# Kernel tuning notes

Hardware: AMD Instinct MI355X
Metric: run time of the kernel (lower is better)

## Reference

```python
import jax, jax.numpy as jnp
import numpy as np
from jax import lax

N = 256
BATCH = 4096
N_MZIS = N * (N - 1) // 2  # 32640


def _reck_positions(n):
    # Static MZI position schedule: for layer in range(n-1): for pos in range(n-1-layer)
    return np.concatenate([np.arange(n - 1 - layer) for layer in range(n - 1)]).astype(np.int32)


def setup_inputs() -> dict:
    key = jax.random.key(0)
    k1, k2, k3, k4 = jax.random.split(key, 4)
    x = jax.random.normal(k1, (BATCH, N), dtype=jnp.float32)
    theta = jax.random.uniform(k2, (N_MZIS,), dtype=jnp.float32) * (np.pi / 2)
    phi_internal = jax.random.uniform(k3, (N_MZIS,), dtype=jnp.float32) * (2 * np.pi)
    phi_external = jax.random.uniform(k4, (N,), dtype=jnp.float32) * (2 * np.pi)
    return {"x": x, "theta": theta, "phi_internal": phi_internal, "phi_external": phi_external}


def _construct_unitary(theta, phi_internal, phi_external):
    n = phi_external.shape[0]
    positions = jnp.asarray(_reck_positions(n))  # [n_mzis], static schedule

    def step(U, inputs):
        pos, th, ph = inputs
        # Extract the two rows touched by this MZI and apply the 2x2 transfer matrix:
        # [[cos,          -sin*e^{-i phi}],
        #  [sin*e^{i phi}, cos          ]]
        rows = lax.dynamic_slice(U, (pos, jnp.int32(0)), (2, n))  # [2, n]
        r0, r1 = rows[0], rows[1]
        c = jnp.cos(th)
        s = jnp.sin(th)
        e = jnp.cos(ph) + 1j * jnp.sin(ph)
        new_rows = jnp.stack([c * r0 - s * jnp.conj(e) * r1,
                              s * e * r0 + c * r1])
        return lax.dynamic_update_slice(U, new_rows, (pos, jnp.int32(0))), None

    U0 = jnp.eye(n, dtype=jnp.complex64)
    U, _ = lax.scan(step, U0, (positions, theta, phi_internal))
    # Final external phase screen: diag(e^{i phi_ext}) @ U
    phase = jnp.cos(phi_external) + 1j * jnp.sin(phi_external)
    return phase[:, None] * U


def reference(x, theta, phi_internal, phi_external):
    U = _construct_unitary(theta, phi_internal, phi_external)  # [N, N] complex64
    out_c = x.astype(jnp.complex64) @ jnp.conj(U).T            # [B, N] complex64
    return jnp.real(out_c).astype(jnp.float32)
```

## Files before the change

### kernel.cpp

```cpp
#include <hip/hip_runtime.h>


#define NN 256
#define NB 4096

typedef float f32x4 __attribute__((ext_vector_type(4)));
typedef short bf16x8 __attribute__((ext_vector_type(8)));

#define WS_AT_OFF   0u
#define WS_BT_OFF   (512u * 1024u)
#define WS_CF_OFF   (1u << 20)
#define WS_PART_OFF (1u << 20)
#define WS_WB_OFF   (3u << 20)
#define WS_XB_OFF   ((3u << 20) + (1u << 19))

__device__ __forceinline__ unsigned short f2bf(float f) {
    unsigned u = __builtin_bit_cast(unsigned, f);
    unsigned r = (u + 0x7FFFu + ((u >> 16) & 1u)) >> 16;
    return (unsigned short)r;
}

__global__ __launch_bounds__(64) void coeff2_kernel(const float* __restrict__ theta,
                                                    const float* __restrict__ phi,
                                                    f32x4* __restrict__ cf3) {
    const int t = blockIdx.x;
    const int l = threadIdx.x;
    const int g = t >> 3, jj = t & 7;
    const int pA = (t & 1) ? (4 * l + 1) : (4 * l);
#pragma unroll
    for (int s = 0; s < 2; ++s) {
        int p = pA + 2 * s;
        f32x4 v = {1.f, 0.f, 0.f, 0.f};
        if (p <= t && p + t <= 508) {
            int L = (t - p) >> 1;
            int k = ((L * (511 - L)) >> 1) + p;
            float st, ct, sp, cp;
            __sincosf(theta[k], &st, &ct);
            __sincosf(phi[k], &sp, &cp);
            v = (f32x4){ct, st * cp, st * sp, 0.f};
        }
        cf3[(g * 16 + 8 * s + jj) * 64 + l] = v;
    }
}

__device__ __forceinline__ float dpp_up1(float x) {
    int r = __builtin_amdgcn_update_dpp(0, __builtin_bit_cast(int, x), 0x138, 0xF, 0xF, true);
    return __builtin_bit_cast(float, r);
}
__device__ __forceinline__ float dpp_dn1(float x) {
    int r = __builtin_amdgcn_update_dpp(0, __builtin_bit_cast(int, x), 0x130, 0xF, 0xF, true);
    return __builtin_bit_cast(float, r);
}

__device__ __forceinline__ void rot2(float& ar, float& ai, float& br, float& bi, f32x4 co) {
    float c = co.x, sx = co.y, sy = co.z;
    float nar = c * ar - (sx * br + sy * bi);
    float nai = c * ai - (sx * bi - sy * br);
    float nbr = sx * ar - sy * ai + c * br;
    float nbi = sx * ai + sy * ar + c * bi;
    ar = nar; ai = nai; br = nbr; bi = nbi;
}

__device__ __forceinline__ void fence() {
    asm volatile("" ::: "memory");
    __builtin_amdgcn_sched_barrier(0);
}

__global__ __launch_bounds__(64, 1) void build_kernel(const f32x4* __restrict__ cf3,
                                                      float2* __restrict__ Ata,
                                                      float2* __restrict__ Btb) {
    const int l  = threadIdx.x;
    const int r0 = 4 * l;
    const int j  = blockIdx.x;
    const int h  = blockIdx.y;
    const int G0 = 32 * h;
    float2* dst = (h ? Ata : Btb) + (size_t)j * NN;

    float ur0 = (r0 + 0 == j) ? 1.f : 0.f, ui0 = 0.f;
    float ur1 = (r0 + 1 == j) ? 1.f : 0.f, ui1 = 0.f;
    float ur2 = (r0 + 2 == j) ? 1.f : 0.f, ui2 = 0.f;
    float ur3 = (r0 + 3 == j) ? 1.f : 0.f, ui3 = 0.f;
    const float lane0_one = (l == 0) ? 1.f : 0.f;

    f32x4 RA[16], RB[16];

    auto loadgrp = [&](int g, f32x4 (&R)[16]) {
        const f32x4* sp = cf3 + (size_t)g * 1024 + l;
#pragma unroll
        for (int s = 0; s < 16; ++s) R[s] = sp[s * 64];
    };

    auto compute = [&](const f32x4 (&R)[16]) {
#pragma unroll
        for (int jj = 0; jj < 8; ++jj) {
            if ((jj & 1) == 0) {
                rot2(ur0, ui0, ur1, ui1, R[jj]);
                rot2(ur2, ui2, ur3, ui3, R[8 + jj]);
            } else {
                float d0r = dpp_dn1(ur0), d0i = dpp_dn1(ui0);
                float u3r = dpp_up1(ur3), u3i = dpp_up1(ui3);
                f32x4 cb = R[8 + jj];
                float cx = dpp_up1(cb.x) + lane0_one;
                float cy = dpp_up1(cb.y);
                float cz = dpp_up1(cb.z);
                rot2(ur1, ui1, ur2, ui2, R[jj]);
                float n3r = cb.x * ur3 - (cb.y * d0r + cb.z * d0i);
                float n3i = cb.x * ui3 - (cb.y * d0i - cb.z * d0r);
                float n0r = cy * u3r - cz * u3i + cx * ur0;
                float n0i = cy * u3i + cz * u3r + cx * ui0;
                ur3 = n3r; ui3 = n3i; ur0 = n0r; ui0 = n0i;
            }
        }
    };

    loadgrp(G0 + 0, RA);
    fence();
    for (int g = 0; g < 32; g += 2) {
        if (g + 1 < 32) loadgrp(G0 + g + 1, RB);
        fence();
        compute(RA);
        if (g + 2 < 32) loadgrp(G0 + g + 2, RA);
        fence();
        compute(RB);
    }

    *(float4*)(dst + r0)     = make_float4(ur0, ui0, ur1, ui1);
    *(float4*)(dst + r0 + 2) = make_float4(ur2, ui2, ur3, ui3);
}

__global__ __launch_bounds__(256) void merge_part_kernel(const float2* __restrict__ At,
                                                         const float2* __restrict__ Bt,
                                                         float2* __restrict__ parts) {
    __shared__ float2 Ats[32][36];
    __shared__ float2 Bts[32][36];

    const int t  = threadIdx.x;
    const int i0 = blockIdx.x * 32;
    const int j0 = blockIdx.y * 32;
    const int kc0 = blockIdx.z * 64;
    const int ti = (t & 15) * 2;
    const int tj = (t >> 4) * 2;

    float sr00 = 0, si00 = 0, sr01 = 0, si01 = 0;
    float sr10 = 0, si10 = 0, sr11 = 0, si11 = 0;

    for (int kc = kc0; kc < kc0 + 64; kc += 32) {
#pragma unroll
        for (int rep = 0; rep < 2; ++rep) {
            int e  = t + rep * 256;
            int kk = e >> 4;
            int f4 = e & 15;
            float4 v = *(const float4*)(At + (size_t)(kc + kk) * NN + i0 + 2 * f4);
            Ats[kk][2 * f4]     = make_float2(v.x, v.y);
            Ats[kk][2 * f4 + 1] = make_float2(v.z, v.w);
            float4 w = *(const float4*)(Bt + (size_t)(j0 + kk) * NN + kc + 2 * f4);
            Bts[kk][2 * f4]     = make_float2(w.x, w.y);
            Bts[kk][2 * f4 + 1] = make_float2(w.z, w.w);
        }
        __syncthreads();
#pragma unroll 8
        for (int k = 0; k < 32; ++k) {
            float2 a0 = Ats[k][ti], a1 = Ats[k][ti + 1];
            float2 b0 = Bts[tj][k], b1 = Bts[tj + 1][k];
            sr00 += a0.x * b0.x - a0.y * b0.y;  si00 += a0.x * b0.y + a0.y * b0.x;
            sr01 += a1.x * b0.x - a1.y * b0.y;  si01 += a1.x * b0.y + a1.y * b0.x;
            sr10 += a0.x * b1.x - a0.y * b1.y;  si10 += a0.x * b1.y + a0.y * b1.x;
            sr11 += a1.x * b1.x - a1.y * b1.y;  si11 += a1.x * b1.y + a1.y * b1.x;
        }
        __syncthreads();
    }

    float2* p = parts + (size_t)blockIdx.z * (NN * NN);
    p[(size_t)(i0 + ti) * NN + j0 + tj]         = make_float2(sr00, si00);
    p[(size_t)(i0 + ti + 1) * NN + j0 + tj]     = make_float2(sr01, si01);
    p[(size_t)(i0 + ti) * NN + j0 + tj + 1]     = make_float2(sr10, si10);
    p[(size_t)(i0 + ti + 1) * NN + j0 + tj + 1] = make_float2(sr11, si11);
}

__global__ __launch_bounds__(256) void reduce_kernel(const float2* __restrict__ parts,
                                                     const float* __restrict__ phi_ext,
                                                     unsigned short* __restrict__ Wb) {
    int gid = blockIdx.x * 256 + threadIdx.x;
    int i  = gid >> 6;
    int j  = (gid & 63) * 4;
    float re0 = 0, im0 = 0, re1 = 0, im1 = 0, re2 = 0, im2 = 0, re3 = 0, im3 = 0;
#pragma unroll
    for (int z = 0; z < 4; ++z) {
        const float2* p = parts + (size_t)z * (NN * NN) + (size_t)i * NN + j;
        float4 a = *(const float4*)(p);
        float4 b = *(const float4*)(p + 2);
        re0 += a.x; im0 += a.y; re1 += a.z; im1 += a.w;
        re2 += b.x; im2 += b.y; re3 += b.z; im3 += b.w;
    }
    float sp, cp;
    __sincosf(phi_ext[i], &sp, &cp);
    ushort4 o;
    o.x = f2bf(cp * re0 - sp * im0);
    o.y = f2bf(cp * re1 - sp * im1);
    o.z = f2bf(cp * re2 - sp * im2);
    o.w = f2bf(cp * re3 - sp * im3);
    *(ushort4*)(Wb + (size_t)i * NN + j) = o;
}

__global__ __launch_bounds__(256) void xb_kernel(const float* __restrict__ x,
                                                 uint4* __restrict__ xb4) {
    int gid = blockIdx.x * 256 + threadIdx.x;
    const float4 v0 = ((const float4*)x)[gid * 2];
    const float4 v1 = ((const float4*)x)[gid * 2 + 1];
    uint4 w;
    w.x = (unsigned)f2bf(v0.x) | ((unsigned)f2bf(v0.y) << 16);
    w.y = (unsigned)f2bf(v0.z) | ((unsigned)f2bf(v0.w) << 16);
    w.z = (unsigned)f2bf(v1.x) | ((unsigned)f2bf(v1.y) << 16);
    w.w = (unsigned)f2bf(v1.z) | ((unsigned)f2bf(v1.w) << 16);
    xb4[gid] = w;
}

__global__ __launch_bounds__(256) void gemm_kernel(const unsigned short* __restrict__ xb,
                                                   const unsigned short* __restrict__ Wb,
                                                   float* __restrict__ out) {
    __shared__ unsigned short Xs[64][72];
    __shared__ unsigned short Ws[64][72];

    const int tid = threadIdx.x;
    const int l   = tid & 63;
    const int wid = tid >> 6;
    const int wm  = wid >> 1, wn = wid & 1;
    const int b0  = blockIdx.x * 64;
    const int i0  = blockIdx.y * 64;

    const int srow = tid >> 2;
    const int sseg = (tid & 3) * 2;

    f32x4 acc[2][2] = {{{0.f, 0.f, 0.f, 0.f}, {0.f, 0.f, 0.f, 0.f}},
                       {{0.f, 0.f, 0.f, 0.f}, {0.f, 0.f, 0.f, 0.f}}};

    const int fr = l & 15;
    const int kg = (l >> 4) * 8;

    for (int k0 = 0; k0 < NN; k0 += 64) {
        uint4 xv  = *(const uint4*)(xb + (size_t)(b0 + srow) * NN + k0 + sseg * 8);
        uint4 wv  = *(const uint4*)(Wb + (size_t)(i0 + srow) * NN + k0 + sseg * 8);
        uint4 xv2 = *(const uint4*)(xb + (size_t)(b0 + srow) * NN + k0 + (sseg + 1) * 8);
        uint4 wv2 = *(const uint4*)(Wb + (size_t)(i0 + srow) * NN + k0 + (sseg + 1) * 8);
        *(uint4*)&Xs[srow][sseg * 8]       = xv;
        *(uint4*)&Ws[srow][sseg * 8]       = wv;
        *(uint4*)&Xs[srow][(sseg + 1) * 8] = xv2;
        *(uint4*)&Ws[srow][(sseg + 1) * 8] = wv2;
        __syncthreads();

#pragma unroll
        for (int ks = 0; ks < 2; ++ks) {
            bf16x8 a0  = *(const bf16x8*)&Xs[wm * 32 + fr][ks * 32 + kg];
            bf16x8 a1  = *(const bf16x8*)&Xs[wm * 32 + 16 + fr][ks * 32 + kg];
            bf16x8 bb0 = *(const bf16x8*)&Ws[wn * 32 + fr][ks * 32 + kg];
            bf16x8 bb1 = *(const bf16x8*)&Ws[wn * 32 + 16 + fr][ks * 32 + kg];
            acc[0][0] = __builtin_amdgcn_mfma_f32_16x16x32_bf16(a0, bb0, acc[0][0], 0, 0, 0);
            acc[0][1] = __builtin_amdgcn_mfma_f32_16x16x32_bf16(a0, bb1, acc[0][1], 0, 0, 0);
            acc[1][0] = __builtin_amdgcn_mfma_f32_16x16x32_bf16(a1, bb0, acc[1][0], 0, 0, 0);
            acc[1][1] = __builtin_amdgcn_mfma_f32_16x16x32_bf16(a1, bb1, acc[1][1], 0, 0, 0);
        }
        __syncthreads();
    }

    const int drow = (l >> 4) * 4;
    const int dcol = l & 15;
#pragma unroll
    for (int mf = 0; mf < 2; ++mf)
#pragma unroll
        for (int nf = 0; nf < 2; ++nf) {
            float* op = out + (size_t)(b0 + wm * 32 + mf * 16 + drow) * NN
                      + i0 + wn * 32 + nf * 16 + dcol;
#pragma unroll
            for (int r = 0; r < 4; ++r) op[(size_t)r * NN] = acc[mf][nf][r];
        }
}

extern "C" void kernel_launch(void* const* d_in, const int* in_sizes, int n_in,
                              void* d_out, int out_size, void* d_ws, size_t ws_size,
                              hipStream_t stream) {
    const float* x     = (const float*)d_in[0];
    const float* theta = (const float*)d_in[1];
    const float* phi_i = (const float*)d_in[2];
    const float* phi_e = (const float*)d_in[3];
    float* out = (float*)d_out;

    float2* At    = (float2*)((char*)d_ws + WS_AT_OFF);
    float2* Bt    = (float2*)((char*)d_ws + WS_BT_OFF);
    f32x4*  cf3   = (f32x4*)((char*)d_ws + WS_CF_OFF);
    float2* parts = (float2*)((char*)d_ws + WS_PART_OFF);
    unsigned short* Wb = (unsigned short*)((char*)d_ws + WS_WB_OFF);
    unsigned short* xb = (unsigned short*)((char*)d_ws + WS_XB_OFF);

    coeff2_kernel<<<dim3(512), dim3(64), 0, stream>>>(theta, phi_i, cf3);
    build_kernel<<<dim3(256, 2), dim3(64), 0, stream>>>(cf3, At, Bt);
    xb_kernel<<<dim3(NB * NN / (256 * 8)), dim3(256), 0, stream>>>(x, (uint4*)xb);
    merge_part_kernel<<<dim3(8, 8, 4), dim3(256), 0, stream>>>(At, Bt, parts);
    reduce_kernel<<<dim3(64), dim3(256), 0, stream>>>(parts, phi_e, Wb);
    gemm_kernel<<<dim3(NB / 64, NN / 64), dim3(256), 0, stream>>>(xb, Wb, out);
}
```

Measured before the change: 48.09 us.

## Fuse x bf16 conversion into GEMM and pack four build waves per block

The separate xb_kernel is removed. The GEMM now loads fp32 x directly and converts it to bf16 while staging into shared memory, which saves one launch and the write and reread of a 2 MB intermediate. build_kernel now runs four waves (four columns) per 256-thread block and adds an s_barrier each iteration, presumably so waves sharing the same coefficient loads stay in lockstep and hit in cache. The cost is that the GEMM reads twice the x bytes per tile, and the barrier can stall waves.

```diff
diff --git a/kernel.cpp b/kernel.cpp
--- a/kernel.cpp
+++ b/kernel.cpp
@@ -12,7 +12,6 @@
 #define WS_CF_OFF   (1u << 20)
 #define WS_PART_OFF (1u << 20)
 #define WS_WB_OFF   (3u << 20)
-#define WS_XB_OFF   ((3u << 20) + (1u << 19))
 
 __device__ __forceinline__ unsigned short f2bf(float f) {
     unsigned u = __builtin_bit_cast(unsigned, f);
@@ -66,14 +65,16 @@
     __builtin_amdgcn_sched_barrier(0);
 }
 
-__global__ __launch_bounds__(64, 1) void build_kernel(const f32x4* __restrict__ cf3,
-                                                      float2* __restrict__ Ata,
-                                                      float2* __restrict__ Btb) {
-    const int l  = threadIdx.x;
-    const int r0 = 4 * l;
-    const int j  = blockIdx.x;
-    const int h  = blockIdx.y;
-    const int G0 = 32 * h;
+__global__ __launch_bounds__(256, 1) void build_kernel(const f32x4* __restrict__ cf3,
+                                                       float2* __restrict__ Ata,
+                                                       float2* __restrict__ Btb) {
+    const int tid = threadIdx.x;
+    const int wid = tid >> 6;
+    const int l   = tid & 63;
+    const int r0  = 4 * l;
+    const int j   = blockIdx.x * 4 + wid;
+    const int h   = blockIdx.y;
+    const int G0  = 32 * h;
     float2* dst = (h ? Ata : Btb) + (size_t)j * NN;
 
     float ur0 = (r0 + 0 == j) ? 1.f : 0.f, ui0 = 0.f;
@@ -122,6 +123,7 @@
         if (g + 2 < 32) loadgrp(G0 + g + 2, RA);
         fence();
         compute(RB);
+        __builtin_amdgcn_s_barrier();
     }
 
     *(float4*)(dst + r0)     = make_float4(ur0, ui0, ur1, ui1);
@@ -202,20 +204,7 @@
     *(ushort4*)(Wb + (size_t)i * NN + j) = o;
 }
 
-__global__ __launch_bounds__(256) void xb_kernel(const float* __restrict__ x,
-                                                 uint4* __restrict__ xb4) {
-    int gid = blockIdx.x * 256 + threadIdx.x;
-    const float4 v0 = ((const float4*)x)[gid * 2];
-    const float4 v1 = ((const float4*)x)[gid * 2 + 1];
-    uint4 w;
-    w.x = (unsigned)f2bf(v0.x) | ((unsigned)f2bf(v0.y) << 16);
-    w.y = (unsigned)f2bf(v0.z) | ((unsigned)f2bf(v0.w) << 16);
-    w.z = (unsigned)f2bf(v1.x) | ((unsigned)f2bf(v1.y) << 16);
-    w.w = (unsigned)f2bf(v1.z) | ((unsigned)f2bf(v1.w) << 16);
-    xb4[gid] = w;
-}
-
-__global__ __launch_bounds__(256) void gemm_kernel(const unsigned short* __restrict__ xb,
+__global__ __launch_bounds__(256) void gemm_kernel(const float* __restrict__ x,
                                                    const unsigned short* __restrict__ Wb,
                                                    float* __restrict__ out) {
     __shared__ unsigned short Xs[64][72];
@@ -238,9 +227,21 @@
     const int kg = (l >> 4) * 8;
 
     for (int k0 = 0; k0 < NN; k0 += 64) {
-        uint4 xv  = *(const uint4*)(xb + (size_t)(b0 + srow) * NN + k0 + sseg * 8);
+        const float* xrow = x + (size_t)(b0 + srow) * NN + k0 + sseg * 8;
+        float4 a = *(const float4*)(xrow);
+        float4 b = *(const float4*)(xrow + 4);
+        float4 c = *(const float4*)(xrow + 8);
+        float4 d = *(const float4*)(xrow + 12);
+        uint4 xv, xv2;
+        xv.x  = (unsigned)f2bf(a.x) | ((unsigned)f2bf(a.y) << 16);
+        xv.y  = (unsigned)f2bf(a.z) | ((unsigned)f2bf(a.w) << 16);
+        xv.z  = (unsigned)f2bf(b.x) | ((unsigned)f2bf(b.y) << 16);
+        xv.w  = (unsigned)f2bf(b.z) | ((unsigned)f2bf(b.w) << 16);
+        xv2.x = (unsigned)f2bf(c.x) | ((unsigned)f2bf(c.y) << 16);
+        xv2.y = (unsigned)f2bf(c.z) | ((unsigned)f2bf(c.w) << 16);
+        xv2.z = (unsigned)f2bf(d.x) | ((unsigned)f2bf(d.y) << 16);
+        xv2.w = (unsigned)f2bf(d.z) | ((unsigned)f2bf(d.w) << 16);
         uint4 wv  = *(const uint4*)(Wb + (size_t)(i0 + srow) * NN + k0 + sseg * 8);
-        uint4 xv2 = *(const uint4*)(xb + (size_t)(b0 + srow) * NN + k0 + (sseg + 1) * 8);
         uint4 wv2 = *(const uint4*)(Wb + (size_t)(i0 + srow) * NN + k0 + (sseg + 1) * 8);
         *(uint4*)&Xs[srow][sseg * 8]       = xv;
         *(uint4*)&Ws[srow][sseg * 8]       = wv;
@@ -289,12 +290,10 @@
     f32x4*  cf3   = (f32x4*)((char*)d_ws + WS_CF_OFF);
     float2* parts = (float2*)((char*)d_ws + WS_PART_OFF);
     unsigned short* Wb = (unsigned short*)((char*)d_ws + WS_WB_OFF);
-    unsigned short* xb = (unsigned short*)((char*)d_ws + WS_XB_OFF);
 
     coeff2_kernel<<<dim3(512), dim3(64), 0, stream>>>(theta, phi_i, cf3);
-    build_kernel<<<dim3(256, 2), dim3(64), 0, stream>>>(cf3, At, Bt);
-    xb_kernel<<<dim3(NB * NN / (256 * 8)), dim3(256), 0, stream>>>(x, (uint4*)xb);
+    build_kernel<<<dim3(64, 2), dim3(256), 0, stream>>>(cf3, At, Bt);
     merge_part_kernel<<<dim3(8, 8, 4), dim3(256), 0, stream>>>(At, Bt, parts);
     reduce_kernel<<<dim3(64), dim3(256), 0, stream>>>(parts, phi_e, Wb);
-    gemm_kernel<<<dim3(NB / 64, NN / 64), dim3(256), 0, stream>>>(xb, Wb, out);
-}
+    gemm_kernel<<<dim3(NB / 64, NN / 64), dim3(256), 0, stream>>>(x, Wb, out);
+}
```

Result: slower. 56.02 us (+16.5%).
